# Optimization experiments

Hardware: AMD Instinct MI355X
Metric: run time of the kernel (lower is better)

## Reference

```python
import jax, jax.numpy as jnp
import numpy as np

D_MODEL = 1024
NUM_HEADS = 16
D_K = D_MODEL // NUM_HEADS


def setup_inputs() -> dict:
    key = jax.random.key(0)
    ks = jax.random.split(key, 12)
    B, S, D = 4, 2048, D_MODEL
    s = 1.0 / np.sqrt(D)
    return {
        "q": jax.random.normal(ks[0], (B, S, D), jnp.float32),
        "k": jax.random.normal(ks[1], (B, S, D), jnp.float32),
        "v": jax.random.normal(ks[2], (B, S, D), jnp.float32),
        "w_q": jax.random.normal(ks[3], (D, D), jnp.float32) * s,
        "b_q": jax.random.normal(ks[4], (D,), jnp.float32) * s,
        "w_k": jax.random.normal(ks[5], (D, D), jnp.float32) * s,
        "b_k": jax.random.normal(ks[6], (D,), jnp.float32) * s,
        "w_v": jax.random.normal(ks[7], (D, D), jnp.float32) * s,
        "b_v": jax.random.normal(ks[8], (D,), jnp.float32) * s,
        "w_0": jax.random.normal(ks[9], (D, D), jnp.float32) * s,
        "b_0": jax.random.normal(ks[10], (D,), jnp.float32) * s,
    }


def reference(q, k, v, w_q, b_q, w_k, b_k, w_v, b_v, w_0, b_0):
    B = q.shape[0]
    H, dk = NUM_HEADS, D_K
    # project and split heads: [B,S,D] -> [B,H,S,dk]
    def split_heads(x):
        return x.reshape(B, -1, H, dk).transpose(0, 2, 1, 3)
    qh = split_heads(q @ w_q + b_q)
    kh = split_heads(k @ w_k + b_k)
    vh = split_heads(v @ w_v + b_v)
    scores = jnp.einsum("bhsd,bhtd->bhst", qh, kh) / np.sqrt(dk).astype(jnp.float32)
    dists = jax.nn.softmax(scores, axis=-1)
    attn = jnp.einsum("bhst,bhtd->bhsd", dists, vh)  # [B,H,S,dk]
    # NOTE: original torch code reshapes WITHOUT transposing heads back
    # (.contiguous().view(B, -1, d_model) on [B,H,S,dk]) -- reproduce faithfully.
    attn = attn.reshape(B, -1, D_MODEL)  # [B,S,D] with head-major interleave
    return attn @ w_0 + b_0
```

## Files before the change

### kernel.cpp

```cpp
#include <hip/hip_runtime.h>
#include <stdint.h>

typedef __bf16 bf16x8 __attribute__((ext_vector_type(8)));
typedef float  f32x4  __attribute__((ext_vector_type(4)));

union U16x8 { uint4 u; uint16_t s[8]; };

__device__ __forceinline__ uint16_t f2b(float f) {
    union { float f; uint32_t u; } c; c.f = f;
    uint32_t u = c.u;
    uint32_t r = u + 0x7fffu + ((u >> 16) & 1u);
    return (uint16_t)(r >> 16);
}

__device__ __forceinline__ uint32_t asu(float f) {
    union { float f; uint32_t u; } c; c.f = f; return c.u;
}
__device__ __forceinline__ uint32_t pack_bf16_hu(float a, float b) {
    uint32_t ua = asu(a) + 0x8000u, ub = asu(b) + 0x8000u;
    return (ua >> 16) | (ub & 0xffff0000u);
}

__device__ __forceinline__ void gl_lds16(const uint16_t* g, uint16_t* l) {
    __builtin_amdgcn_global_load_lds(
        (const __attribute__((address_space(1))) void*)g,
        (__attribute__((address_space(3))) void*)l, 16, 0, 0);
}

__global__ void cast3_f32_bf16(const float* __restrict__ x0, const float* __restrict__ x1,
                               const float* __restrict__ x2,
                               uint16_t* __restrict__ y0, uint16_t* __restrict__ y1,
                               uint16_t* __restrict__ y2, int n4) {
    const float* x; uint16_t* y;
    switch (blockIdx.y) {
        case 0: x = x0; y = y0; break;
        case 1: x = x1; y = y1; break;
        default: x = x2; y = y2; break;
    }
    int i = blockIdx.x * blockDim.x + threadIdx.x;
    if (i < n4) {
        float4 v = ((const float4*)x)[i];
        ushort4 o;
        o.x = f2b(v.x); o.y = f2b(v.y); o.z = f2b(v.z); o.w = f2b(v.w);
        *(ushort4*)(y + (size_t)i * 4) = o;
    }
}

__global__ void transpose_cast4(const float* __restrict__ W0, const float* __restrict__ W1,
                                const float* __restrict__ W2, const float* __restrict__ W3,
                                uint16_t* __restrict__ O0, uint16_t* __restrict__ O1,
                                uint16_t* __restrict__ O2, uint16_t* __restrict__ O3) {
    __shared__ float tile[64][65];
    const float* W; uint16_t* Wt;
    switch (blockIdx.z) {
        case 0: W = W0; Wt = O0; break;
        case 1: W = W1; Wt = O1; break;
        case 2: W = W2; Wt = O2; break;
        default: W = W3; Wt = O3; break;
    }
    const int k0 = blockIdx.y * 64, n0 = blockIdx.x * 64;
    const int tx = threadIdx.x & 63, ty = threadIdx.x >> 6;
    #pragma unroll
    for (int r = ty; r < 64; r += 4)
        tile[r][tx] = W[(size_t)(k0 + r) * 1024 + n0 + tx];
    __syncthreads();
    #pragma unroll
    for (int r = ty; r < 64; r += 4)
        Wt[(size_t)(n0 + r) * 1024 + k0 + tx] = f2b(tile[tx][r]);
}

__global__ __launch_bounds__(256, 3)
void gemm_qkv(const uint16_t* __restrict__ A0, const uint16_t* __restrict__ A1,
              const uint16_t* __restrict__ A2,
              const uint16_t* __restrict__ B0, const uint16_t* __restrict__ B1,
              const uint16_t* __restrict__ B2,
              const float* __restrict__ c0, const float* __restrict__ c1,
              const float* __restrict__ c2,
              uint16_t* __restrict__ O0, uint16_t* __restrict__ O1,
              uint16_t* __restrict__ O2, float qscale) {
    __shared__ uint16_t SH[2 * 128 * 32] __attribute__((aligned(16)));
    uint16_t* As = SH;
    uint16_t* Bs = SH + 128 * 32;

    const uint16_t* A; const uint16_t* Bt; const float* bias; uint16_t* Cout; float scale;
    switch (blockIdx.z) {
        case 0: A = A0; Bt = B0; bias = c0; Cout = O0; scale = qscale; break;
        case 1: A = A1; Bt = B1; bias = c1; Cout = O1; scale = 1.0f;  break;
        default: A = A2; Bt = B2; bias = c2; Cout = O2; scale = 1.0f; break;
    }

    const int tid = threadIdx.x;
    const int m0 = blockIdx.y * 128, n0 = blockIdx.x * 128;
    const int l = tid & 63, ln = l & 15, qd = l >> 4;
    const int w = tid >> 6;
    const int wm = (w >> 1) * 64, wn = (w & 1) * 64;

    f32x4 acc[4][4] = {};

    for (int kk = 0; kk < 1024; kk += 32) {
        __syncthreads();
        #pragma unroll
        for (int i = 0; i < 2; i++) {
            int c = tid + i * 256;
            gl_lds16(&A[(size_t)(m0 + (c >> 2)) * 1024 + kk + (c & 3) * 8], &As[c * 8]);
            gl_lds16(&Bt[(size_t)(n0 + (c >> 2)) * 1024 + kk + (c & 3) * 8], &Bs[c * 8]);
        }
        __syncthreads();

        bf16x8 af[4], bfr[4];
        #pragma unroll
        for (int i = 0; i < 4; i++)
            af[i] = *(const bf16x8*)&As[(wm + i * 16 + ln) * 32 + qd * 8];
        #pragma unroll
        for (int j = 0; j < 4; j++)
            bfr[j] = *(const bf16x8*)&Bs[(wn + j * 16 + ln) * 32 + qd * 8];
        #pragma unroll
        for (int i = 0; i < 4; i++)
            #pragma unroll
            for (int j = 0; j < 4; j++)
                acc[i][j] = __builtin_amdgcn_mfma_f32_16x16x32_bf16(af[i], bfr[j], acc[i][j], 0, 0, 0);
    }

    float bv[4];
    #pragma unroll
    for (int j = 0; j < 4; j++) bv[j] = bias[n0 + wn + j * 16 + ln];

    __syncthreads();
    uint16_t* scr = (uint16_t*)SH + w * 1024;
    const int colb = n0 + wn;
    const int h = colb >> 6;
    #pragma unroll
    for (int i = 0; i < 4; i++) {
        #pragma unroll
        for (int j = 0; j < 4; j++)
            #pragma unroll
            for (int r = 0; r < 4; r++)
                scr[(qd * 4 + r) * 64 + j * 16 + ln] = f2b((acc[i][j][r] + bv[j]) * scale);
        #pragma unroll
        for (int ii = 0; ii < 2; ii++) {
            int ch = ii * 64 + l, row = ch >> 3, sg = ch & 7;
            int grow = m0 + wm + i * 16 + row;
            int b = grow >> 11, s = grow & 2047;
            *(uint4*)&Cout[(size_t)((b * 16 + h) * 2048 + s) * 64 + sg * 8] =
                *(uint4*)&scr[row * 64 + sg * 8];
        }
    }
}

__global__ __launch_bounds__(256, 3)
void gemm_o(const uint16_t* __restrict__ A, const uint16_t* __restrict__ Bt,
            const float* __restrict__ bias, float* __restrict__ Cout) {
    __shared__ uint16_t SH[2 * 128 * 32] __attribute__((aligned(16)));
    uint16_t* As = SH;
    uint16_t* Bs = SH + 128 * 32;

    const int tid = threadIdx.x;
    const int m0 = blockIdx.y * 128, n0 = blockIdx.x * 128;
    const int l = tid & 63, ln = l & 15, qd = l >> 4;
    const int w = tid >> 6;
    const int wm = (w >> 1) * 64, wn = (w & 1) * 64;

    f32x4 acc[4][4] = {};

    for (int kk = 0; kk < 1024; kk += 32) {
        __syncthreads();
        #pragma unroll
        for (int i = 0; i < 2; i++) {
            int c = tid + i * 256;
            gl_lds16(&A[(size_t)(m0 + (c >> 2)) * 1024 + kk + (c & 3) * 8], &As[c * 8]);
            gl_lds16(&Bt[(size_t)(n0 + (c >> 2)) * 1024 + kk + (c & 3) * 8], &Bs[c * 8]);
        }
        __syncthreads();

        bf16x8 af[4], bfr[4];
        #pragma unroll
        for (int i = 0; i < 4; i++)
            af[i] = *(const bf16x8*)&As[(wm + i * 16 + ln) * 32 + qd * 8];
        #pragma unroll
        for (int j = 0; j < 4; j++)
            bfr[j] = *(const bf16x8*)&Bs[(wn + j * 16 + ln) * 32 + qd * 8];
        #pragma unroll
        for (int i = 0; i < 4; i++)
            #pragma unroll
            for (int j = 0; j < 4; j++)
                acc[i][j] = __builtin_amdgcn_mfma_f32_16x16x32_bf16(af[i], bfr[j], acc[i][j], 0, 0, 0);
    }

    float bv[4];
    #pragma unroll
    for (int j = 0; j < 4; j++) bv[j] = bias[n0 + wn + j * 16 + ln];

    __syncthreads();
    float* scr = (float*)SH + w * 1024;
    #pragma unroll
    for (int i = 0; i < 4; i++) {
        #pragma unroll
        for (int j = 0; j < 4; j++)
            #pragma unroll
            for (int r = 0; r < 4; r++)
                scr[(qd * 4 + r) * 64 + j * 16 + ln] = acc[i][j][r] + bv[j];
        #pragma unroll
        for (int ii = 0; ii < 4; ii++) {
            int ch = ii * 64 + l, row = ch >> 4, sg = ch & 15;
            *(float4*)&Cout[(size_t)(m0 + wm + i * 16 + row) * 1024 + n0 + wn + sg * 4] =
                *(float4*)&scr[row * 64 + sg * 4];
        }
    }
}

__global__ __launch_bounds__(512, 4)
void attn_kernel(const uint16_t* __restrict__ Qh, const uint16_t* __restrict__ Kh,
                 const uint16_t* __restrict__ Vh, uint16_t* __restrict__ Of) {
    __shared__ uint16_t Ks[2][64 * 64] __attribute__((aligned(16)));
    __shared__ uint16_t Vt[2][64 * 72] __attribute__((aligned(16)));
    __shared__ uint16_t Ps[256 * 72]   __attribute__((aligned(16)));

    const int tid = threadIdx.x;
    const int w = tid >> 6, l = tid & 63, ln = l & 15, qd = l >> 4;
    const size_t base = (size_t)blockIdx.y * 131072;
    const int q0 = blockIdx.x * 256;

    const int krow = tid >> 3;
    const int kchunk = (tid & 7) ^ (krow & 7);
    const int swz0 = ((0 + qd) ^ (ln & 7)) * 8;
    const int swz1 = ((4 + qd) ^ (ln & 7)) * 8;
    const int vu = tid & 31, vsg = tid >> 5;

    bf16x8 qf[2][2];
    #pragma unroll
    for (int tq = 0; tq < 2; tq++)
        #pragma unroll
        for (int ks = 0; ks < 2; ks++)
            qf[tq][ks] = *(const bf16x8*)&Qh[base + (size_t)(q0 + w * 32 + tq * 16 + ln) * 64 + ks * 32 + qd * 8];

    f32x4 oacc[2][4] = {};
    float mrun[2] = { -__builtin_inff(), -__builtin_inff() };
    float lrun[2] = { 0.f, 0.f };

    gl_lds16(&Kh[base + (size_t)krow * 64 + kchunk * 8], &Ks[0][tid * 8]);
    if (w < 4) {
        uint4 vr0 = *(const uint4*)&Vh[base + (size_t)(2 * vu) * 64 + vsg * 8];
        uint4 vr1 = *(const uint4*)&Vh[base + (size_t)(2 * vu + 1) * 64 + vsg * 8];
        U16x8 a, b; a.u = vr0; b.u = vr1;
        #pragma unroll
        for (int e = 0; e < 8; e++) {
            uint32_t pk = (uint32_t)a.s[e] | ((uint32_t)b.s[e] << 16);
            *(uint32_t*)&Vt[0][(vsg * 8 + e) * 72 + 2 * vu] = pk;
        }
    }

    for (int j = 0; j < 32; j++) {
        const int cur = j & 1, nxt = cur ^ 1;
        __syncthreads();

        if (j < 31) {
            const int t0n = (j + 1) * 64;
            if (w < 4) {
                uint4 vr0 = *(const uint4*)&Vh[base + (size_t)(t0n + 2 * vu) * 64 + vsg * 8];
                uint4 vr1 = *(const uint4*)&Vh[base + (size_t)(t0n + 2 * vu + 1) * 64 + vsg * 8];
                gl_lds16(&Kh[base + (size_t)(t0n + krow) * 64 + kchunk * 8], &Ks[nxt][tid * 8]);
                U16x8 a, b; a.u = vr0; b.u = vr1;
                #pragma unroll
                for (int e = 0; e < 8; e++) {
                    uint32_t pk = (uint32_t)a.s[e] | ((uint32_t)b.s[e] << 16);
                    *(uint32_t*)&Vt[nxt][(vsg * 8 + e) * 72 + 2 * vu] = pk;
                }
            } else {
                gl_lds16(&Kh[base + (size_t)(t0n + krow) * 64 + kchunk * 8], &Ks[nxt][tid * 8]);
            }
        }

        f32x4 sa[4][2] = {};
        __builtin_amdgcn_s_setprio(1);
        #pragma unroll
        for (int tt = 0; tt < 4; tt++) {
            bf16x8 kb0 = *(const bf16x8*)&Ks[cur][(tt * 16 + ln) * 64 + swz0];
            bf16x8 kb1 = *(const bf16x8*)&Ks[cur][(tt * 16 + ln) * 64 + swz1];
            #pragma unroll
            for (int tq = 0; tq < 2; tq++) {
                sa[tt][tq] = __builtin_amdgcn_mfma_f32_16x16x32_bf16(kb0, qf[tq][0], sa[tt][tq], 0, 0, 0);
                sa[tt][tq] = __builtin_amdgcn_mfma_f32_16x16x32_bf16(kb1, qf[tq][1], sa[tt][tq], 0, 0, 0);
            }
        }
        __builtin_amdgcn_s_setprio(0);

        #pragma unroll
        for (int tq = 0; tq < 2; tq++) {
            float a0 = fmaxf(fmaxf(sa[0][tq][0], sa[0][tq][1]), fmaxf(sa[0][tq][2], sa[0][tq][3]));
            float a1 = fmaxf(fmaxf(sa[1][tq][0], sa[1][tq][1]), fmaxf(sa[1][tq][2], sa[1][tq][3]));
            float a2 = fmaxf(fmaxf(sa[2][tq][0], sa[2][tq][1]), fmaxf(sa[2][tq][2], sa[2][tq][3]));
            float a3 = fmaxf(fmaxf(sa[3][tq][0], sa[3][tq][1]), fmaxf(sa[3][tq][2], sa[3][tq][3]));
            float mx = fmaxf(fmaxf(a0, a1), fmaxf(a2, a3));
            mx = fmaxf(mx, __shfl_xor(mx, 16));
            mx = fmaxf(mx, __shfl_xor(mx, 32));
            if (!__all(mx - mrun[tq] <= 8.0f)) {
                float mnew = fmaxf(mrun[tq], mx);
                float al = __builtin_amdgcn_exp2f(mrun[tq] - mnew);
                mrun[tq] = mnew;
                lrun[tq] *= al;
                #pragma unroll
                for (int dt = 0; dt < 4; dt++)
                    #pragma unroll
                    for (int r = 0; r < 4; r++) oacc[tq][dt][r] *= al;
            }
            const float m = mrun[tq];
            float rs = 0.f;
            #pragma unroll
            for (int tt = 0; tt < 4; tt++) {
                float p0 = __builtin_amdgcn_exp2f(sa[tt][tq][0] - m);
                float p1 = __builtin_amdgcn_exp2f(sa[tt][tq][1] - m);
                float p2 = __builtin_amdgcn_exp2f(sa[tt][tq][2] - m);
                float p3 = __builtin_amdgcn_exp2f(sa[tt][tq][3] - m);
                rs += (p0 + p1) + (p2 + p3);
                uint2 pk;
                pk.x = pack_bf16_hu(p0, p1);
                pk.y = pack_bf16_hu(p2, p3);
                *(uint2*)&Ps[(w * 32 + tq * 16 + ln) * 72 + tt * 16 + qd * 4] = pk;
            }
            rs += __shfl_xor(rs, 16);
            rs += __shfl_xor(rs, 32);
            lrun[tq] += rs;
        }

        bf16x8 pa[2][2];
        #pragma unroll
        for (int tq = 0; tq < 2; tq++)
            #pragma unroll
            for (int ks = 0; ks < 2; ks++)
                pa[tq][ks] = *(const bf16x8*)&Ps[(w * 32 + tq * 16 + ln) * 72 + ks * 32 + qd * 8];
        __builtin_amdgcn_s_setprio(1);
        #pragma unroll
        for (int dtp = 0; dtp < 2; dtp++) {
            bf16x8 vb[2][2];
            #pragma unroll
            for (int dh = 0; dh < 2; dh++)
                #pragma unroll
                for (int ks = 0; ks < 2; ks++)
                    vb[dh][ks] = *(const bf16x8*)&Vt[cur][((dtp * 2 + dh) * 16 + ln) * 72 + ks * 32 + qd * 8];
            #pragma unroll
            for (int tq = 0; tq < 2; tq++)
                #pragma unroll
                for (int dh = 0; dh < 2; dh++)
                    #pragma unroll
                    for (int ks = 0; ks < 2; ks++)
                        oacc[tq][dtp * 2 + dh] = __builtin_amdgcn_mfma_f32_16x16x32_bf16(
                            vb[dh][ks], pa[tq][ks], oacc[tq][dtp * 2 + dh], 0, 0, 0);
        }
        __builtin_amdgcn_s_setprio(0);
    }

    #pragma unroll
    for (int tq = 0; tq < 2; tq++) {
        float inv = 1.0f / lrun[tq];
        #pragma unroll
        for (int dt = 0; dt < 4; dt++) {
            uint2 pk;
            pk.x = pack_bf16_hu(oacc[tq][dt][0] * inv, oacc[tq][dt][1] * inv);
            pk.y = pack_bf16_hu(oacc[tq][dt][2] * inv, oacc[tq][dt][3] * inv);
            *(uint2*)&Ps[(w * 32 + tq * 16 + ln) * 72 + dt * 16 + qd * 4] = pk;
        }
    }
    __syncthreads();
    #pragma unroll
    for (int i = 0; i < 4; i++) {
        int c = tid + i * 512, row = c >> 3, sg = c & 7;
        *(uint4*)&Of[base + (size_t)(q0 + row) * 64 + sg * 8] =
            *(const uint4*)&Ps[row * 72 + sg * 8];
    }
}

extern "C" void kernel_launch(void* const* d_in, const int* in_sizes, int n_in,
                              void* d_out, int out_size, void* d_ws, size_t ws_size,
                              hipStream_t stream) {
    const float* q   = (const float*)d_in[0];
    const float* k   = (const float*)d_in[1];
    const float* v   = (const float*)d_in[2];
    const float* w_q = (const float*)d_in[3];
    const float* b_q = (const float*)d_in[4];
    const float* w_k = (const float*)d_in[5];
    const float* b_k = (const float*)d_in[6];
    const float* w_v = (const float*)d_in[7];
    const float* b_v = (const float*)d_in[8];
    const float* w_0 = (const float*)d_in[9];
    const float* b_0 = (const float*)d_in[10];

    uint16_t* ws  = (uint16_t*)d_ws;
    const size_t WE = 1048576, NE = 8388608;
    uint16_t* wtq = ws;
    uint16_t* wtk = wtq + WE;
    uint16_t* wtv = wtk + WE;
    uint16_t* wt0 = wtv + WE;
    uint16_t* xq  = wt0 + WE;
    uint16_t* xk  = xq + NE;
    uint16_t* xv  = xk + NE;
    uint16_t* Qh  = xv + NE;
    uint16_t* Kh  = Qh + NE;
    uint16_t* Vh  = Kh + NE;
    uint16_t* Pf  = xq;

    const dim3 tb(256);
    const dim3 gT(16, 16, 4);
    const dim3 gC(8192, 3);
    const dim3 gQ(8, 64, 3);
    const dim3 gO(8, 64);
    const dim3 gA(8, 64);
    const int  n4 = 2097152;

    const float qscale = 0.125f * 1.44269504f;

    transpose_cast4<<<gT, tb, 0, stream>>>(w_q, w_k, w_v, w_0, wtq, wtk, wtv, wt0);
    cast3_f32_bf16<<<gC, tb, 0, stream>>>(q, k, v, xq, xk, xv, n4);
    gemm_qkv<<<gQ, tb, 0, stream>>>(xq, xk, xv, wtq, wtk, wtv, b_q, b_k, b_v,
                                    Qh, Kh, Vh, qscale);
    attn_kernel<<<gA, dim3(512), 0, stream>>>(Qh, Kh, Vh, Pf);
    gemm_o<<<gO, tb, 0, stream>>>(Pf, wt0, b_0, (float*)d_out);
}
```

Measured before the change: 381.4 us.

## Double per-wave query tile in attention kernel to amortize K/V tile loads

Each wave now processes 64 query rows instead of 32, so a block covers 512 queries and the grid halves to 4x64 blocks. Every K/V tile staged in LDS is reused across twice as many query rows, which cuts LDS fragment reads and global K/V traffic per unit of work. The P staging buffer shrinks to one 16-row slab per wave, reused for each query sub-tile, and the output write-back is done per sub-tile with extra barriers. In exchange, register pressure roughly doubles, the launch bound is relaxed to 2 blocks, and 256 blocks give fewer waves to hide latency.

```diff
diff --git a/kernel.cpp b/kernel.cpp
--- a/kernel.cpp
+++ b/kernel.cpp
@@ -208,17 +208,17 @@
     }
 }
 
-__global__ __launch_bounds__(512, 4)
+__global__ __launch_bounds__(512, 2)
 void attn_kernel(const uint16_t* __restrict__ Qh, const uint16_t* __restrict__ Kh,
                  const uint16_t* __restrict__ Vh, uint16_t* __restrict__ Of) {
     __shared__ uint16_t Ks[2][64 * 64] __attribute__((aligned(16)));
     __shared__ uint16_t Vt[2][64 * 72] __attribute__((aligned(16)));
-    __shared__ uint16_t Ps[256 * 72]   __attribute__((aligned(16)));
+    __shared__ uint16_t Ps[128 * 72]   __attribute__((aligned(16)));
 
     const int tid = threadIdx.x;
     const int w = tid >> 6, l = tid & 63, ln = l & 15, qd = l >> 4;
     const size_t base = (size_t)blockIdx.y * 131072;
-    const int q0 = blockIdx.x * 256;
+    const int q0 = blockIdx.x * 512;
 
     const int krow = tid >> 3;
     const int kchunk = (tid & 7) ^ (krow & 7);
@@ -226,16 +226,16 @@
     const int swz1 = ((4 + qd) ^ (ln & 7)) * 8;
     const int vu = tid & 31, vsg = tid >> 5;
 
-    bf16x8 qf[2][2];
-    #pragma unroll
-    for (int tq = 0; tq < 2; tq++)
+    bf16x8 qf[4][2];
+    #pragma unroll
+    for (int tq = 0; tq < 4; tq++)
         #pragma unroll
         for (int ks = 0; ks < 2; ks++)
-            qf[tq][ks] = *(const bf16x8*)&Qh[base + (size_t)(q0 + w * 32 + tq * 16 + ln) * 64 + ks * 32 + qd * 8];
-
-    f32x4 oacc[2][4] = {};
-    float mrun[2] = { -__builtin_inff(), -__builtin_inff() };
-    float lrun[2] = { 0.f, 0.f };
+            qf[tq][ks] = *(const bf16x8*)&Qh[base + (size_t)(q0 + w * 64 + tq * 16 + ln) * 64 + ks * 32 + qd * 8];
+
+    f32x4 oacc[4][4] = {};
+    float mrun[4] = { -__builtin_inff(), -__builtin_inff(), -__builtin_inff(), -__builtin_inff() };
+    float lrun[4] = { 0.f, 0.f, 0.f, 0.f };
 
     gl_lds16(&Kh[base + (size_t)krow * 64 + kchunk * 8], &Ks[0][tid * 8]);
     if (w < 4) {
@@ -270,22 +270,23 @@
             }
         }
 
-        f32x4 sa[4][2] = {};
+        f32x4 sa[4][4] = {};
         __builtin_amdgcn_s_setprio(1);
         #pragma unroll
         for (int tt = 0; tt < 4; tt++) {
             bf16x8 kb0 = *(const bf16x8*)&Ks[cur][(tt * 16 + ln) * 64 + swz0];
             bf16x8 kb1 = *(const bf16x8*)&Ks[cur][(tt * 16 + ln) * 64 + swz1];
             #pragma unroll
-            for (int tq = 0; tq < 2; tq++) {
+            for (int tq = 0; tq < 4; tq++) {
                 sa[tt][tq] = __builtin_amdgcn_mfma_f32_16x16x32_bf16(kb0, qf[tq][0], sa[tt][tq], 0, 0, 0);
                 sa[tt][tq] = __builtin_amdgcn_mfma_f32_16x16x32_bf16(kb1, qf[tq][1], sa[tt][tq], 0, 0, 0);
             }
         }
         __builtin_amdgcn_s_setprio(0);
 
-        #pragma unroll
-        for (int tq = 0; tq < 2; tq++) {
+        bf16x8 pa[4][2];
+        #pragma unroll
+        for (int tq = 0; tq < 4; tq++) {
             float a0 = fmaxf(fmaxf(sa[0][tq][0], sa[0][tq][1]), fmaxf(sa[0][tq][2], sa[0][tq][3]));
             float a1 = fmaxf(fmaxf(sa[1][tq][0], sa[1][tq][1]), fmaxf(sa[1][tq][2], sa[1][tq][3]));
             float a2 = fmaxf(fmaxf(sa[2][tq][0], sa[2][tq][1]), fmaxf(sa[2][tq][2], sa[2][tq][3]));
@@ -315,57 +316,48 @@
                 uint2 pk;
                 pk.x = pack_bf16_hu(p0, p1);
                 pk.y = pack_bf16_hu(p2, p3);
-                *(uint2*)&Ps[(w * 32 + tq * 16 + ln) * 72 + tt * 16 + qd * 4] = pk;
+                *(uint2*)&Ps[(w * 16 + ln) * 72 + tt * 16 + qd * 4] = pk;
             }
             rs += __shfl_xor(rs, 16);
             rs += __shfl_xor(rs, 32);
             lrun[tq] += rs;
-        }
-
-        bf16x8 pa[2][2];
-        #pragma unroll
-        for (int tq = 0; tq < 2; tq++)
-            #pragma unroll
-            for (int ks = 0; ks < 2; ks++)
-                pa[tq][ks] = *(const bf16x8*)&Ps[(w * 32 + tq * 16 + ln) * 72 + ks * 32 + qd * 8];
+            pa[tq][0] = *(const bf16x8*)&Ps[(w * 16 + ln) * 72 + 0 * 32 + qd * 8];
+            pa[tq][1] = *(const bf16x8*)&Ps[(w * 16 + ln) * 72 + 1 * 32 + qd * 8];
+        }
+
         __builtin_amdgcn_s_setprio(1);
         #pragma unroll
-        for (int dtp = 0; dtp < 2; dtp++) {
-            bf16x8 vb[2][2];
-            #pragma unroll
-            for (int dh = 0; dh < 2; dh++)
-                #pragma unroll
-                for (int ks = 0; ks < 2; ks++)
-                    vb[dh][ks] = *(const bf16x8*)&Vt[cur][((dtp * 2 + dh) * 16 + ln) * 72 + ks * 32 + qd * 8];
-            #pragma unroll
-            for (int tq = 0; tq < 2; tq++)
-                #pragma unroll
-                for (int dh = 0; dh < 2; dh++)
-                    #pragma unroll
-                    for (int ks = 0; ks < 2; ks++)
-                        oacc[tq][dtp * 2 + dh] = __builtin_amdgcn_mfma_f32_16x16x32_bf16(
-                            vb[dh][ks], pa[tq][ks], oacc[tq][dtp * 2 + dh], 0, 0, 0);
+        for (int dt = 0; dt < 4; dt++) {
+            bf16x8 vb0 = *(const bf16x8*)&Vt[cur][(dt * 16 + ln) * 72 + 0 * 32 + qd * 8];
+            bf16x8 vb1 = *(const bf16x8*)&Vt[cur][(dt * 16 + ln) * 72 + 1 * 32 + qd * 8];
+            #pragma unroll
+            for (int tq = 0; tq < 4; tq++) {
+                oacc[tq][dt] = __builtin_amdgcn_mfma_f32_16x16x32_bf16(vb0, pa[tq][0], oacc[tq][dt], 0, 0, 0);
+                oacc[tq][dt] = __builtin_amdgcn_mfma_f32_16x16x32_bf16(vb1, pa[tq][1], oacc[tq][dt], 0, 0, 0);
+            }
         }
         __builtin_amdgcn_s_setprio(0);
     }
 
     #pragma unroll
-    for (int tq = 0; tq < 2; tq++) {
+    for (int tq = 0; tq < 4; tq++) {
         float inv = 1.0f / lrun[tq];
         #pragma unroll
         for (int dt = 0; dt < 4; dt++) {
             uint2 pk;
             pk.x = pack_bf16_hu(oacc[tq][dt][0] * inv, oacc[tq][dt][1] * inv);
             pk.y = pack_bf16_hu(oacc[tq][dt][2] * inv, oacc[tq][dt][3] * inv);
-            *(uint2*)&Ps[(w * 32 + tq * 16 + ln) * 72 + dt * 16 + qd * 4] = pk;
-        }
-    }
-    __syncthreads();
-    #pragma unroll
-    for (int i = 0; i < 4; i++) {
-        int c = tid + i * 512, row = c >> 3, sg = c & 7;
-        *(uint4*)&Of[base + (size_t)(q0 + row) * 64 + sg * 8] =
-            *(const uint4*)&Ps[row * 72 + sg * 8];
+            *(uint2*)&Ps[(w * 16 + ln) * 72 + dt * 16 + qd * 4] = pk;
+        }
+        __syncthreads();
+        #pragma unroll
+        for (int i = 0; i < 2; i++) {
+            int c = tid + i * 512, row = c >> 3, sg = c & 7;
+            int qrow = q0 + (row >> 4) * 64 + tq * 16 + (row & 15);
+            *(uint4*)&Of[base + (size_t)qrow * 64 + sg * 8] =
+                *(const uint4*)&Ps[row * 72 + sg * 8];
+        }
+        __syncthreads();
     }
 }
 
@@ -403,7 +395,7 @@
     const dim3 gC(8192, 3);
     const dim3 gQ(8, 64, 3);
     const dim3 gO(8, 64);
-    const dim3 gA(8, 64);
+    const dim3 gA(4, 64);
     const int  n4 = 2097152;
 
     const float qscale = 0.125f * 1.44269504f;
```

After: 390.1 us. +2.3%, slower.
